# Kernel tuning notes

Measured on AMD Instinct MI355X. Metric: run time of the kernel, lower is better.

The kernel has to match this reference:

```python
import jax, jax.numpy as jnp
import numpy as np

T, B, D, H = 1024, 8, 1024, 16
NH = D // H  # 64, per-head width (nhid)
W_SCALE = 0.02


def setup_inputs() -> dict:
    key = jax.random.key(0)
    ks = jax.random.split(key, 10)
    return {
        "input_tensor": jax.random.normal(ks[0], (T, B, D), jnp.float32),
        "keys_vector": jax.random.normal(ks[1], (T, B, D), jnp.float32),
        "values_vector": jax.random.normal(ks[2], (T, B, D), jnp.float32),
        # per-head projection weights: [H, D, NH]
        "Wq": jax.random.normal(ks[3], (H, D, NH), jnp.float32) * W_SCALE,
        "bq": jnp.zeros((H, NH), jnp.float32),
        "Wk": jax.random.normal(ks[4], (H, D, NH), jnp.float32) * W_SCALE,
        "bk": jnp.zeros((H, NH), jnp.float32),
        "Wv": jax.random.normal(ks[5], (H, D, NH), jnp.float32) * W_SCALE,
        "bv": jnp.zeros((H, NH), jnp.float32),
        # output projection after concatenating heads
        "Wo": jax.random.normal(ks[6], (D, D), jnp.float32) * W_SCALE,
        "bo": jnp.zeros((D,), jnp.float32),
        "mask": 1,  # True: causal (growing key slice per timestep)
    }


def reference(input_tensor, keys_vector, values_vector, Wq, bq, Wk, bk, Wv, bv, Wo, bo, mask):
    # Vectorized equivalent of the per-timestep loop: query at step t attends
    # to keys/values[:t+1] when mask is set, else to the full sequence.
    q = jnp.einsum('tbd,hdk->tbhk', input_tensor, Wq) + bq   # [T,B,H,NH]
    k = jnp.einsum('sbd,hdk->sbhk', keys_vector, Wk) + bk    # [T,B,H,NH]
    v = jnp.einsum('sbd,hdk->sbhk', values_vector, Wv) + bv  # [T,B,H,NH]

    scale = 1.0 / jnp.sqrt(jnp.float32(NH))
    scores = jnp.einsum('tbhk,sbhk->bhts', q, k) * scale     # [B,H,T,T]
    if mask:
        causal = jnp.tril(jnp.ones((T, T), dtype=bool))      # s <= t
        scores = jnp.where(causal[None, None], scores, jnp.float32(-1e9))
    attn = jax.nn.softmax(scores, axis=-1)                   # over key dim s

    out = jnp.einsum('bhts,sbhk->tbhk', attn, v)             # [T,B,H,NH]
    out = out.reshape(T, B, D)                               # concat heads
    return out @ Wo.T + bo                                   # [T,B,D]
```

## Files before the change

### kernel.cpp

```cpp
#include <hip/hip_runtime.h>

typedef short bf16x8 __attribute__((ext_vector_type(8)));
typedef float f32x4 __attribute__((ext_vector_type(4)));
typedef float f32x16 __attribute__((ext_vector_type(16)));

typedef const __attribute__((address_space(1))) void* gptr_t;
typedef __attribute__((address_space(3))) void* sptr_t;

#define Z16 {0.f,0.f,0.f,0.f,0.f,0.f,0.f,0.f,0.f,0.f,0.f,0.f,0.f,0.f,0.f,0.f}

__device__ __forceinline__ void glds16(const void* g, void* s) {
  __builtin_amdgcn_global_load_lds((gptr_t)g, (sptr_t)s, 16, 0, 0);
}

__device__ __forceinline__ unsigned short f2bf(float x) {
  unsigned u = __float_as_uint(x);
  u = u + 0x7fffu + ((u >> 16) & 1u);
  return (unsigned short)(u >> 16);
}

__device__ __forceinline__ unsigned packbf(float lo, float hi) {
  return (unsigned)f2bf(lo) | (((unsigned)f2bf(hi)) << 16);
}

__global__ __launch_bounds__(256) void prep(const float* __restrict__ X,
                                            const float* __restrict__ KY,
                                            const float* __restrict__ VY,
                                            const float* __restrict__ Wo,
                                            const float* __restrict__ Wq,
                                            const float* __restrict__ Wk,
                                            const float* __restrict__ Wv,
                                            unsigned short* __restrict__ XB,
                                            unsigned short* __restrict__ WOB,
                                            unsigned short* __restrict__ WT) {
  __shared__ float tile[64][65];
  if (blockIdx.x < 2048) {
    int stride = 2048 * 256;
    for (int i = blockIdx.x * 256 + threadIdx.x; i < 6553600; i += stride) {
      const float* in; unsigned short* out; int k;
      if (i < 2097152)      { in = X;  out = XB;            k = i; }
      else if (i < 4194304) { in = KY; out = XB + 8388608;  k = i - 2097152; }
      else if (i < 6291456) { in = VY; out = XB + 16777216; k = i - 4194304; }
      else                  { in = Wo; out = WOB;           k = i - 6291456; }
      float4 v = ((const float4*)in)[k];
      uint2 r;
      r.x = packbf(v.x, v.y);
      r.y = packbf(v.z, v.w);
      ((uint2*)out)[k] = r;
    }
    return;
  }
  int idx = blockIdx.x - 2048;
  int bx = idx & 15, by = idx >> 4;
  int m = by >> 4, h = by & 15, d0 = bx * 64;
  const float* src = (m == 0 ? Wq : (m == 1 ? Wk : Wv)) + (size_t)h * 65536;
  int c = (threadIdx.x & 15) * 4, r0 = threadIdx.x >> 4;
#pragma unroll
  for (int rr = 0; rr < 4; ++rr) {
    int dr = rr * 16 + r0;
    float4 v = *(const float4*)(src + (size_t)(d0 + dr) * 64 + c);
    tile[dr][c + 0] = v.x; tile[dr][c + 1] = v.y;
    tile[dr][c + 2] = v.z; tile[dr][c + 3] = v.w;
  }
  __syncthreads();
#pragma unroll
  for (int rr = 0; rr < 4; ++rr) {
    int kr = rr * 16 + r0;
    uint2 pk;
    pk.x = packbf(tile[c + 0][kr], tile[c + 1][kr]);
    pk.y = packbf(tile[c + 2][kr], tile[c + 3][kr]);
    *(uint2*)(WT + ((size_t)(m * 1024 + h * 64 + kr)) * 1024 + d0 + c) = pk;
  }
}

__global__ __launch_bounds__(256) void gemm_qkv(const unsigned short* __restrict__ Ab,
                                                const unsigned short* __restrict__ Bb,
                                                const float* __restrict__ bi0,
                                                const float* __restrict__ bi1,
                                                const float* __restrict__ bi2,
                                                unsigned short* __restrict__ outp) {
  const int K = 1024;
  int z = blockIdx.z;
  const unsigned short* A = Ab + (size_t)z * 8192 * 1024;
  const unsigned short* BT = Bb + (size_t)z * 1024 * 1024;
  const float* bias = z == 0 ? bi0 : (z == 1 ? bi1 : bi2);
  int lin = blockIdx.y * 64 + blockIdx.x;
  int mt = (lin & 7) * 8 + ((lin >> 3) & 7);
  int nt = lin >> 6;
  int m0 = mt * 128, n0 = nt * 128;
  __shared__ __align__(16) char lds[65536];
  int tid = threadIdx.x, w = tid >> 6, l = tid & 63, ml = l & 15, hi = l >> 4;
  int wr = (w >> 1) * 64, wc = (w & 1) * 64;
  int srow = l >> 3;
  int kphys = (l & 7) << 4;
  f32x4 acc[4][4] = {};
#pragma unroll
  for (int i = 0; i < 4; ++i) {
    int c = w * 4 + i;
    int row = c * 8 + srow;
    int klog = kphys ^ ((row & 7) << 4);
    glds16((const char*)(A + (size_t)(m0 + row) * K) + klog, lds + c * 1024);
    glds16((const char*)(BT + (size_t)(n0 + row) * K) + klog, lds + 16384 + c * 1024);
  }
  __syncthreads();
  int cur = 0;
  for (int kt16 = 0; kt16 < 16; ++kt16) {
    if (kt16 + 1 < 16) {
      char* nb = lds + (cur ^ 1) * 32768;
      int kt = (kt16 + 1) * 64;
#pragma unroll
      for (int i = 0; i < 4; ++i) {
        int c = w * 4 + i;
        int row = c * 8 + srow;
        int klog = kphys ^ ((row & 7) << 4);
        glds16((const char*)(A + (size_t)(m0 + row) * K + kt) + klog, nb + c * 1024);
        glds16((const char*)(BT + (size_t)(n0 + row) * K + kt) + klog, nb + 16384 + c * 1024);
      }
    }
    char* As = lds + cur * 32768;
    char* Bs = As + 16384;
#pragma unroll
    for (int ks = 0; ks < 2; ++ks) {
      bf16x8 af[4], bfr[4];
#pragma unroll
      for (int mi = 0; mi < 4; ++mi) {
        int row = wr + mi * 16 + ml;
        af[mi] = *(const bf16x8*)(As + row * 128 + ((ks * 64 + (hi << 4)) ^ ((row & 7) << 4)));
      }
#pragma unroll
      for (int ni = 0; ni < 4; ++ni) {
        int row = wc + ni * 16 + ml;
        bfr[ni] = *(const bf16x8*)(Bs + row * 128 + ((ks * 64 + (hi << 4)) ^ ((row & 7) << 4)));
      }
      __builtin_amdgcn_s_setprio(1);
#pragma unroll
      for (int mi = 0; mi < 4; ++mi)
#pragma unroll
        for (int ni = 0; ni < 4; ++ni)
          acc[mi][ni] = __builtin_amdgcn_mfma_f32_16x16x32_bf16(af[mi], bfr[ni], acc[mi][ni], 0, 0, 0);
      __builtin_amdgcn_s_setprio(0);
    }
    __syncthreads();
    cur ^= 1;
  }
#pragma unroll
  for (int mi = 0; mi < 4; ++mi) {
#pragma unroll
    for (int ni = 0; ni < 4; ++ni) {
      int col = wc + ni * 16 + ml;
      float bv = bias[n0 + col];
#pragma unroll
      for (int r = 0; r < 4; ++r) {
        int row = wr + mi * 16 + (hi << 2) + r;
        float v = acc[mi][ni][r] + bv;
        float pv = __shfl_xor(v, 1);
        unsigned pk = (ml & 1) ? packbf(pv, v) : packbf(v, pv);
        *(unsigned*)(lds + row * 256 + (((col * 2) & ~3) ^ ((row & 7) << 4))) = pk;
      }
    }
  }
  __syncthreads();
  unsigned short* ob = outp + (size_t)z * 8388608;
  if (z != 2) {
    int rr = tid >> 1, hh = tid & 1;
    int t = (m0 + rr) >> 3, b = (m0 + rr) & 7;
    int hg = (n0 >> 6) + hh;
    unsigned short* dst = ob + (size_t)(b * 16 + hg) * 65536 + (size_t)t * 64;
#pragma unroll
    for (int j = 0; j < 8; ++j) {
      uint4 d = *(uint4*)(lds + rr * 256 + ((hh * 128 + j * 16) ^ ((rr & 7) << 4)));
      *(uint4*)(dst + j * 8) = d;
    }
  } else {
    int t0 = m0 >> 3;
#pragma unroll
    for (int q = 0; q < 4; ++q) {
      int run = q * 256 + tid;
      int k = run & 63;
      int bh2 = run >> 6;
      int b = bh2 >> 1, hh = bh2 & 1;
      int colb = (hh * 64 + k) * 2;
      union { unsigned short u[16]; uint4 v[2]; } tmp;
#pragma unroll
      for (int tp = 0; tp < 16; ++tp) {
        int rowt = tp * 8 + b;
        tmp.u[tp] = *(unsigned short*)(lds + rowt * 256 + (colb ^ ((b & 7) << 4)));
      }
      int hg = (n0 >> 6) + hh;
      unsigned short* dst = ob + (size_t)(b * 16 + hg) * 65536 + (size_t)k * 1024 + t0;
      *(uint4*)dst = tmp.v[0];
      *(uint4*)(dst + 8) = tmp.v[1];
    }
  }
}

__global__ __launch_bounds__(256) void gemm_out(const unsigned short* __restrict__ A,
                                                const unsigned short* __restrict__ BT,
                                                const float* __restrict__ bias,
                                                float* __restrict__ outp) {
  const int K = 1024;
  int lin = blockIdx.y * 64 + blockIdx.x;
  int mt = (lin & 7) * 8 + ((lin >> 3) & 7);
  int nt = lin >> 6;
  int m0 = mt * 128, n0 = nt * 128;
  __shared__ __align__(16) char lds[65536];
  int tid = threadIdx.x, w = tid >> 6, l = tid & 63, ml = l & 15, hi = l >> 4;
  int wr = (w >> 1) * 64, wc = (w & 1) * 64;
  int srow = l >> 3;
  int kphys = (l & 7) << 4;
  f32x4 acc[4][4] = {};
#pragma unroll
  for (int i = 0; i < 4; ++i) {
    int c = w * 4 + i;
    int row = c * 8 + srow;
    int klog = kphys ^ ((row & 7) << 4);
    glds16((const char*)(A + (size_t)(m0 + row) * K) + klog, lds + c * 1024);
    glds16((const char*)(BT + (size_t)(n0 + row) * K) + klog, lds + 16384 + c * 1024);
  }
  __syncthreads();
  int cur = 0;
  for (int kt16 = 0; kt16 < 16; ++kt16) {
    if (kt16 + 1 < 16) {
      char* nb = lds + (cur ^ 1) * 32768;
      int kt = (kt16 + 1) * 64;
#pragma unroll
      for (int i = 0; i < 4; ++i) {
        int c = w * 4 + i;
        int row = c * 8 + srow;
        int klog = kphys ^ ((row & 7) << 4);
        glds16((const char*)(A + (size_t)(m0 + row) * K + kt) + klog, nb + c * 1024);
        glds16((const char*)(BT + (size_t)(n0 + row) * K + kt) + klog, nb + 16384 + c * 1024);
      }
    }
    char* As = lds + cur * 32768;
    char* Bs = As + 16384;
#pragma unroll
    for (int ks = 0; ks < 2; ++ks) {
      bf16x8 af[4], bfr[4];
#pragma unroll
      for (int mi = 0; mi < 4; ++mi) {
        int row = wr + mi * 16 + ml;
        af[mi] = *(const bf16x8*)(As + row * 128 + ((ks * 64 + (hi << 4)) ^ ((row & 7) << 4)));
      }
#pragma unroll
      for (int ni = 0; ni < 4; ++ni) {
        int row = wc + ni * 16 + ml;
        bfr[ni] = *(const bf16x8*)(Bs + row * 128 + ((ks * 64 + (hi << 4)) ^ ((row & 7) << 4)));
      }
      __builtin_amdgcn_s_setprio(1);
#pragma unroll
      for (int mi = 0; mi < 4; ++mi)
#pragma unroll
        for (int ni = 0; ni < 4; ++ni)
          acc[mi][ni] = __builtin_amdgcn_mfma_f32_16x16x32_bf16(af[mi], bfr[ni], acc[mi][ni], 0, 0, 0);
      __builtin_amdgcn_s_setprio(0);
    }
    __syncthreads();
    cur ^= 1;
  }
#pragma unroll
  for (int mi = 0; mi < 4; ++mi) {
#pragma unroll
    for (int ni = 0; ni < 4; ++ni) {
      int col = n0 + wc + ni * 16 + ml;
      float bv = bias[col];
#pragma unroll
      for (int r = 0; r < 4; ++r) {
        int row = m0 + wr + mi * 16 + (hi << 2) + r;
        outp[(size_t)row * 1024 + col] = acc[mi][ni][r] + bv;
      }
    }
  }
}

__global__ __launch_bounds__(512, 4) void attn_k(const unsigned short* __restrict__ Qp,
                                                 const unsigned short* __restrict__ Kp,
                                                 const unsigned short* __restrict__ VTp,
                                                 unsigned short* __restrict__ Op,
                                                 const int* __restrict__ maskp) {
  int lin = blockIdx.x;
  int xcd = lin & 7, idx = lin >> 3;
  int bh = xcd + 8 * (idx >> 2);
  int j = idx & 3;
  const size_t base = (size_t)bh * 65536;
  int tid = threadIdx.x, w = tid >> 6, l = tid & 63;
  int ml5 = l & 31, hi1 = l >> 5;
  int half = w & 1, pi = w >> 1;
  int stripe = (pi == 0) ? j : (pi == 1) ? (15 - j) : (pi == 2) ? (7 - j) : (8 + j);
  int tw0 = stripe * 64 + half * 32;
  int t_glob = tw0 + ml5;
  int msk = *maskp;
  const float CE = 0.18033688011112042f;
  bf16x8 bq[4];
#pragma unroll
  for (int kd = 0; kd < 4; ++kd)
    bq[kd] = *(const bf16x8*)(Qp + base + (size_t)t_glob * 64 + kd * 16 + hi1 * 8);
  f32x16 o0 = Z16, o1 = Z16;
  float m_run = -3e38f, l_run = 0.f;
  int lim = msk ? stripe : 15;
  const unsigned short* krow = Kp + base + (size_t)ml5 * 64 + hi1 * 8;
  const unsigned short* vrow = VTp + base + (size_t)ml5 * 1024 + hi1 * 8;
  for (int st = 0; st <= lim; ++st) {
    f32x16 s0 = Z16, s1 = Z16;
    const unsigned short* ka = krow + st * 4096;
    __builtin_amdgcn_s_setprio(1);
#pragma unroll
    for (int kd = 0; kd < 4; ++kd) {
      bf16x8 a0 = *(const bf16x8*)(ka + kd * 16);
      bf16x8 a1 = *(const bf16x8*)(ka + 2048 + kd * 16);
      s0 = __builtin_amdgcn_mfma_f32_32x32x16_bf16(a0, bq[kd], s0, 0, 0, 0);
      s1 = __builtin_amdgcn_mfma_f32_32x32x16_bf16(a1, bq[kd], s1, 0, 0, 0);
    }
    __builtin_amdgcn_s_setprio(0);
    if (msk && st == stripe) {
#pragma unroll
      for (int r = 0; r < 16; ++r) {
        int sl = st * 64 + (r & 3) + 8 * (r >> 2) + 4 * hi1;
        if (sl > t_glob) s0[r] = -1e30f;
        if (sl + 32 > t_glob) s1[r] = -1e30f;
      }
    }
    float t8[8];
#pragma unroll
    for (int r = 0; r < 8; ++r)
      t8[r] = fmaxf(fmaxf(s0[r], s0[r + 8]), fmaxf(s1[r], s1[r + 8]));
    float tm = fmaxf(fmaxf(fmaxf(t8[0], t8[1]), fmaxf(t8[2], t8[3])),
                     fmaxf(fmaxf(t8[4], t8[5]), fmaxf(t8[6], t8[7])));
    tm = fmaxf(tm, __shfl_xor(tm, 32));
    if (!__all(tm <= m_run + 8.0f)) {
      float m_new = fmaxf(m_run, tm);
      float sc2 = exp2f((m_run - m_new) * CE);
      l_run *= sc2;
#pragma unroll
      for (int r = 0; r < 16; ++r) { o0[r] *= sc2; o1[r] *= sc2; }
      m_run = m_new;
    }
    float mC = m_run * CE;
#pragma unroll
    for (int r = 0; r < 16; ++r) {
      s0[r] = exp2f(fmaf(s0[r], CE, -mC));
      s1[r] = exp2f(fmaf(s1[r], CE, -mC));
    }
    float a8[8];
#pragma unroll
    for (int r = 0; r < 8; ++r)
      a8[r] = (s0[r] + s0[r + 8]) + (s1[r] + s1[r + 8]);
    float ps = ((a8[0] + a8[1]) + (a8[2] + a8[3])) + ((a8[4] + a8[5]) + (a8[6] + a8[7]));
    ps += __shfl_xor(ps, 32);
    l_run += ps;
    unsigned cc0[4][2], cc1[4][2];
#pragma unroll
    for (int q = 0; q < 4; ++q) {
      cc0[q][0] = packbf(s0[4 * q + 0], s0[4 * q + 1]);
      cc0[q][1] = packbf(s0[4 * q + 2], s0[4 * q + 3]);
      cc1[q][0] = packbf(s1[4 * q + 0], s1[4 * q + 1]);
      cc1[q][1] = packbf(s1[4 * q + 2], s1[4 * q + 3]);
    }
#define CCa(a, p) ((a) < 4 ? cc0[(a) & 3][p] : cc1[(a) & 3][p])
    union U4 { unsigned u[4]; bf16x8 v; };
    bf16x8 pb[4];
#pragma unroll
    for (int kb = 0; kb < 4; ++kb) {
      U4 t;
#pragma unroll
      for (int p = 0; p < 2; ++p) {
        unsigned x = CCa(2 * kb, p), y = CCa(2 * kb + 1, p);
        unsigned v = hi1 ? x : y;
        unsigned wv = hi1 ? y : x;
        unsigned vs = __shfl_xor(v, 32);
        t.u[p]     = hi1 ? vs : wv;
        t.u[2 + p] = hi1 ? wv : vs;
      }
      pb[kb] = t.v;
    }
#undef CCa
    const unsigned short* va = vrow + st * 64;
    __builtin_amdgcn_s_setprio(1);
#pragma unroll
    for (int kb = 0; kb < 4; ++kb) {
      bf16x8 v0 = *(const bf16x8*)(va + kb * 16);
      bf16x8 v1 = *(const bf16x8*)(va + 32768 + kb * 16);
      o0 = __builtin_amdgcn_mfma_f32_32x32x16_bf16(v0, pb[kb], o0, 0, 0, 0);
      o1 = __builtin_amdgcn_mfma_f32_32x32x16_bf16(v1, pb[kb], o1, 0, 0, 0);
    }
    __builtin_amdgcn_s_setprio(0);
  }
  float rl = 1.0f / l_run;
  int b = bh >> 4, h = bh & 15;
  unsigned short* orow = Op + (size_t)(t_glob * 8 + b) * 1024 + h * 64;
#pragma unroll
  for (int q2 = 0; q2 < 4; ++q2) {
    uint2 pk0, pk1;
    pk0.x = packbf(o0[4 * q2 + 0] * rl, o0[4 * q2 + 1] * rl);
    pk0.y = packbf(o0[4 * q2 + 2] * rl, o0[4 * q2 + 3] * rl);
    *(uint2*)(orow + 4 * hi1 + 8 * q2) = pk0;
    pk1.x = packbf(o1[4 * q2 + 0] * rl, o1[4 * q2 + 1] * rl);
    pk1.y = packbf(o1[4 * q2 + 2] * rl, o1[4 * q2 + 3] * rl);
    *(uint2*)(orow + 32 + 4 * hi1 + 8 * q2) = pk1;
  }
}

extern "C" void kernel_launch(void* const* d_in, const int* in_sizes, int n_in,
                              void* d_out, int out_size, void* d_ws, size_t ws_size,
                              hipStream_t stream) {
  const float* X  = (const float*)d_in[0];
  const float* KY = (const float*)d_in[1];
  const float* VY = (const float*)d_in[2];
  const float* Wq = (const float*)d_in[3];
  const float* bq = (const float*)d_in[4];
  const float* Wk = (const float*)d_in[5];
  const float* bk = (const float*)d_in[6];
  const float* Wv = (const float*)d_in[7];
  const float* bv = (const float*)d_in[8];
  const float* Wo = (const float*)d_in[9];
  const float* bo = (const float*)d_in[10];
  const int* mask = (const int*)d_in[11];
  char* ws = (char*)d_ws;
  unsigned short* XB  = (unsigned short*)(ws);
  unsigned short* WT  = (unsigned short*)(ws + 48ll * 1024 * 1024);
  unsigned short* WOB = (unsigned short*)(ws + 54ll * 1024 * 1024);
  unsigned short* QP  = (unsigned short*)(ws + 56ll * 1024 * 1024);
  unsigned short* OP  = (unsigned short*)(ws + 104ll * 1024 * 1024);

  prep<<<2816, 256, 0, stream>>>(X, KY, VY, Wo, Wq, Wk, Wv, XB, WOB, WT);
  gemm_qkv<<<dim3(64, 8, 3), 256, 0, stream>>>(XB, WT, bq, bk, bv, QP);
  attn_k<<<512, 512, 0, stream>>>(QP, QP + 8388608, QP + 16777216, OP, mask);
  gemm_out<<<dim3(64, 8, 1), 256, 0, stream>>>(OP, WOB, bo, (float*)d_out);
}
```

Baseline: 211.3 us.

## Stage K/V tiles through double-buffered swizzled LDS in smaller attention blocks

The attention kernel moves from 512-thread blocks, where each wave streamed K and V straight from global memory, to 128-thread blocks covering one 64-query stripe each. The two waves share K/V tiles loaded asynchronously into double-buffered, XOR-swizzled LDS, with the next tile prefetched while the current one is computed. The aim is to cut redundant global/L2 traffic and hide load latency behind the MFMA work. The cost is per-tile block barriers, the loss of the old pairing that balanced causal workloads within a block, and a heavier-first ordering of stripes across the grid.

Result: faster. 185.5 us, median of 2 (-12.2%).

```diff
diff --git a/kernel.cpp b/kernel.cpp
--- a/kernel.cpp
+++ b/kernel.cpp
@@ -8,6 +8,10 @@
 typedef __attribute__((address_space(3))) void* sptr_t;
 
 #define Z16 {0.f,0.f,0.f,0.f,0.f,0.f,0.f,0.f,0.f,0.f,0.f,0.f,0.f,0.f,0.f,0.f}
+#define VMCNT(n) asm volatile("s_waitcnt vmcnt(" #n ")" ::: "memory")
+#define LGKM0 asm volatile("s_waitcnt lgkmcnt(0)" ::: "memory")
+#define SCHEDB __builtin_amdgcn_sched_barrier(0)
+#define SBAR __builtin_amdgcn_s_barrier()
 
 __device__ __forceinline__ void glds16(const void* g, void* s) {
   __builtin_amdgcn_global_load_lds((gptr_t)g, (sptr_t)s, 16, 0, 0);
@@ -273,22 +277,21 @@
   }
 }
 
-__global__ __launch_bounds__(512, 4) void attn_k(const unsigned short* __restrict__ Qp,
+__global__ __launch_bounds__(128, 2) void attn_k(const unsigned short* __restrict__ Qp,
                                                  const unsigned short* __restrict__ Kp,
                                                  const unsigned short* __restrict__ VTp,
                                                  unsigned short* __restrict__ Op,
                                                  const int* __restrict__ maskp) {
   int lin = blockIdx.x;
   int xcd = lin & 7, idx = lin >> 3;
-  int bh = xcd + 8 * (idx >> 2);
-  int j = idx & 3;
+  int bh = xcd + 8 * (idx & 15);
+  int s = 15 - (idx >> 4);
   const size_t base = (size_t)bh * 65536;
   int tid = threadIdx.x, w = tid >> 6, l = tid & 63;
   int ml5 = l & 31, hi1 = l >> 5;
-  int half = w & 1, pi = w >> 1;
-  int stripe = (pi == 0) ? j : (pi == 1) ? (15 - j) : (pi == 2) ? (7 - j) : (8 + j);
-  int tw0 = stripe * 64 + half * 32;
+  int tw0 = s * 64 + w * 32;
   int t_glob = tw0 + ml5;
+  __shared__ __align__(16) char lds[32768];
   int msk = *maskp;
   const float CE = 0.18033688011112042f;
   bf16x8 bq[4];
@@ -297,22 +300,59 @@
     bq[kd] = *(const bf16x8*)(Qp + base + (size_t)t_glob * 64 + kd * 16 + hi1 * 8);
   f32x16 o0 = Z16, o1 = Z16;
   float m_run = -3e38f, l_run = 0.f;
-  int lim = msk ? stripe : 15;
-  const unsigned short* krow = Kp + base + (size_t)ml5 * 64 + hi1 * 8;
-  const unsigned short* vrow = VTp + base + (size_t)ml5 * 1024 + hi1 * 8;
+  int lim = msk ? s : 15;
+  int srow = l >> 3, kphys = (l & 7) << 4;
+  int klog = kphys ^ (srow << 4);
+  int swz = (ml5 & 7) << 4;
+  if (w == 0) {
+#pragma unroll
+    for (int i = 0; i < 8; ++i) {
+      int row = i * 8 + srow;
+      glds16((const char*)(Kp + base + (size_t)row * 64) + klog, lds + i * 1024);
+    }
+  } else {
+#pragma unroll
+    for (int i = 0; i < 8; ++i) {
+      int row = i * 8 + srow;
+      glds16((const char*)(VTp + base + (size_t)row * 1024) + klog, lds + 8192 + i * 1024);
+    }
+  }
+  int cur = 0;
   for (int st = 0; st <= lim; ++st) {
+    if (st < lim) {
+      char* nb = lds + (cur ^ 1) * 16384;
+      if (w == 0) {
+#pragma unroll
+        for (int i = 0; i < 8; ++i) {
+          int row = i * 8 + srow;
+          glds16((const char*)(Kp + base + (size_t)((st + 1) * 64 + row) * 64) + klog, nb + i * 1024);
+        }
+      } else {
+#pragma unroll
+        for (int i = 0; i < 8; ++i) {
+          int row = i * 8 + srow;
+          glds16((const char*)(VTp + base + (size_t)row * 1024 + (st + 1) * 64) + klog, nb + 8192 + i * 1024);
+        }
+      }
+      VMCNT(8);
+    } else {
+      VMCNT(0);
+    }
+    SCHEDB; SBAR; SCHEDB;
+    char* Ks = lds + cur * 16384;
+    char* Vs = Ks + 8192;
     f32x16 s0 = Z16, s1 = Z16;
-    const unsigned short* ka = krow + st * 4096;
     __builtin_amdgcn_s_setprio(1);
 #pragma unroll
     for (int kd = 0; kd < 4; ++kd) {
-      bf16x8 a0 = *(const bf16x8*)(ka + kd * 16);
-      bf16x8 a1 = *(const bf16x8*)(ka + 2048 + kd * 16);
+      int koff = kd * 32 + hi1 * 16;
+      bf16x8 a0 = *(const bf16x8*)(Ks + ml5 * 128 + (koff ^ swz));
+      bf16x8 a1 = *(const bf16x8*)(Ks + (32 + ml5) * 128 + (koff ^ swz));
       s0 = __builtin_amdgcn_mfma_f32_32x32x16_bf16(a0, bq[kd], s0, 0, 0, 0);
       s1 = __builtin_amdgcn_mfma_f32_32x32x16_bf16(a1, bq[kd], s1, 0, 0, 0);
     }
     __builtin_amdgcn_s_setprio(0);
-    if (msk && st == stripe) {
+    if (msk && st == s) {
 #pragma unroll
       for (int r = 0; r < 16; ++r) {
         int sl = st * 64 + (r & 3) + 8 * (r >> 2) + 4 * hi1;
@@ -374,16 +414,18 @@
       pb[kb] = t.v;
     }
 #undef CCa
-    const unsigned short* va = vrow + st * 64;
     __builtin_amdgcn_s_setprio(1);
 #pragma unroll
     for (int kb = 0; kb < 4; ++kb) {
-      bf16x8 v0 = *(const bf16x8*)(va + kb * 16);
-      bf16x8 v1 = *(const bf16x8*)(va + 32768 + kb * 16);
+      int koff = kb * 32 + hi1 * 16;
+      bf16x8 v0 = *(const bf16x8*)(Vs + ml5 * 128 + (koff ^ swz));
+      bf16x8 v1 = *(const bf16x8*)(Vs + (32 + ml5) * 128 + (koff ^ swz));
       o0 = __builtin_amdgcn_mfma_f32_32x32x16_bf16(v0, pb[kb], o0, 0, 0, 0);
       o1 = __builtin_amdgcn_mfma_f32_32x32x16_bf16(v1, pb[kb], o1, 0, 0, 0);
     }
     __builtin_amdgcn_s_setprio(0);
+    SCHEDB; LGKM0; SBAR;
+    cur ^= 1;
   }
   float rl = 1.0f / l_run;
   int b = bh >> 4, h = bh & 15;
@@ -424,6 +466,6 @@
 
   prep<<<2816, 256, 0, stream>>>(X, KY, VY, Wo, Wq, Wk, Wv, XB, WOB, WT);
   gemm_qkv<<<dim3(64, 8, 3), 256, 0, stream>>>(XB, WT, bq, bk, bv, QP);
-  attn_k<<<512, 512, 0, stream>>>(QP, QP + 8388608, QP + 16777216, OP, mask);
+  attn_k<<<2048, 128, 0, stream>>>(QP, QP + 8388608, QP + 16777216, OP, mask);
   gemm_out<<<dim3(64, 8, 1), 256, 0, stream>>>(OP, WOB, bo, (float*)d_out);
 }
```
